# Optimization experiments

Hardware: AMD Instinct MI355X
Metric: run time of the kernel (lower is better)

## Reference

```python
import jax, jax.numpy as jnp
import numpy as np

B, L_SRC, H = 16, 2048, 1024


def setup_inputs() -> dict:
    key = jax.random.key(0)
    ks = jax.random.split(key, 12)
    s = 1.0 / np.sqrt(H)
    return {
        "query": jax.random.normal(ks[0], (B, 1, H), jnp.float32),
        "states": jax.random.normal(ks[1], (B, L_SRC, H), jnp.float32),
        "states_features": jax.random.normal(ks[2], (B, L_SRC, H), jnp.float32),
        "coverage": jax.random.uniform(ks[3], (B, L_SRC, 1), jnp.float32),
        "source_mask": jax.random.randint(ks[4], (B, L_SRC), 0, 2, jnp.int32),
        "is_coverage": 1,
        "Wq": jax.random.normal(ks[5], (H, H), jnp.float32) * s,
        "bq": jax.random.normal(ks[6], (H,), jnp.float32) * s,
        "Wc": jax.random.normal(ks[7], (1, H), jnp.float32) * s,
        "v": jax.random.normal(ks[8], (H, 1), jnp.float32) * s,
        "Wout": jax.random.normal(ks[9], (H, 2 * H), jnp.float32) * s,
        "bout": jax.random.normal(ks[10], (H,), jnp.float32) * s,
    }


def reference(query, states, states_features, coverage, source_mask, is_coverage,
              Wq, bq, Wc, v, Wout, bout):
    # query: (B,1,H); states/states_features: (B,L,H); coverage: (B,L,1)
    query_features = query @ Wq.T + bq                       # (B,1,H), broadcasts over L
    total = query_features + states_features                 # (B,L,H)
    if is_coverage:
        total = total + coverage @ Wc                        # Linear(1,H), no bias
    alignments = jnp.tanh(total) @ v                         # (B,L,1)
    mask = source_mask.astype(bool)[:, :, None]              # (B,L,1)
    alignments = jnp.where(mask, alignments, -jnp.inf)
    align_vectors = jax.nn.softmax(alignments, axis=1)       # softmax over L_src
    c = jnp.einsum('bls,blh->bsh', align_vectors, states)    # (B,1,H)
    concat_c = jnp.concatenate([c, query], axis=2)           # (B,1,2H)
    attn_h = concat_c @ Wout.T + bout                         # (B,1,H)
    new_coverage = coverage + align_vectors
    return attn_h, new_coverage, align_vectors
```

## Files before the change

kernel.cpp:

```cpp
#include <hip/hip_runtime.h>
#include <cfloat>

#define HD 1024
#define LS 2048
#define NB 16
#define LCHUNK 64
#define LPER   (LS / LCHUNK)

struct f4 { float x, y, z, w; };

__device__ inline f4 ld4(const float* p) { return *reinterpret_cast<const f4*>(p); }

__device__ inline float ftanh(float x) {
    x = fminf(10.f, fmaxf(-10.f, x));
    float t = __expf(2.f * x);
    return 1.f - 2.f * __builtin_amdgcn_rcpf(t + 1.f);
}

__device__ inline float dotTanh(const f4& s, const f4& q, const f4& wc, const f4& v, float covs) {
    return ftanh(s.x + q.x + covs * wc.x) * v.x
         + ftanh(s.y + q.y + covs * wc.y) * v.y
         + ftanh(s.z + q.z + covs * wc.z) * v.z
         + ftanh(s.w + q.w + covs * wc.w) * v.w;
}

__device__ inline float waveReduce(float v) {
    #pragma unroll
    for (int off = 32; off; off >>= 1) v += __shfl_xor(v, off, 64);
    return v;
}

__global__ void qf_kernel(const float* __restrict__ query, const float* __restrict__ Wq,
                          const float* __restrict__ bq, float* __restrict__ qf) {
    int h = blockIdx.x;
    int tid = threadIdx.x;
    int wv = tid >> 6, lane = tid & 63;
    int k0 = tid * 4;
    f4 w = ld4(Wq + (size_t)h * HD + k0);
    __shared__ float red[4][NB];
    float acc[NB];
    #pragma unroll
    for (int b = 0; b < NB; ++b) {
        f4 q = ld4(query + b * HD + k0);
        acc[b] = w.x * q.x + w.y * q.y + w.z * q.z + w.w * q.w;
    }
    #pragma unroll
    for (int b = 0; b < NB; ++b) {
        float r = waveReduce(acc[b]);
        if (lane == 0) red[wv][b] = r;
    }
    __syncthreads();
    if (tid < NB) {
        float s = red[0][tid] + red[1][tid] + red[2][tid] + red[3][tid];
        qf[tid * HD + h] = s + bq[h];
    }
}

__global__ __launch_bounds__(256) void fusedEC_kernel(
    const float* __restrict__ sf, const float* __restrict__ qf,
    const float* __restrict__ Wc, const float* __restrict__ vv,
    const float* __restrict__ coverage, const int* __restrict__ mask,
    const int* __restrict__ is_cov_p, const float* __restrict__ states,
    float* __restrict__ e_out, float* __restrict__ cpart)
{
    int chunk = blockIdx.x;
    int b = blockIdx.y;
    int tid = threadIdx.x;
    int wv = tid >> 6, lane = tid & 63;
    int l4 = lane * 4;
    int base_row = b * LS + chunk * LPER;
    int row0 = base_row + wv * 8;

    __shared__ float e_loc[LPER];

    int covflag = *is_cov_p;
    int4 mk0 = *reinterpret_cast<const int4*>(mask + row0);
    int4 mk1 = *reinterpret_cast<const int4*>(mask + row0 + 4);
    bool m[8] = { mk0.x != 0, mk0.y != 0, mk0.z != 0, mk0.w != 0,
                  mk1.x != 0, mk1.y != 0, mk1.z != 0, mk1.w != 0 };
    float cov[8];
    #pragma unroll
    for (int r = 0; r < 8; ++r) cov[r] = (covflag && m[r]) ? coverage[row0 + r] : 0.f;

    const float* qfr = qf + b * HD + l4;
    const float* ps = sf + (size_t)row0 * HD + l4;
    float acc[8] = {0.f, 0.f, 0.f, 0.f, 0.f, 0.f, 0.f, 0.f};

    #pragma unroll
    for (int it = 0; it < 4; ++it) {
        int o = it * 256;
        f4 q  = ld4(qfr + o);
        f4 wc = ld4(Wc + o + l4);
        f4 vf = ld4(vv + o + l4);
        f4 s[8];
        #pragma unroll
        for (int r = 0; r < 8; ++r) if (m[r]) s[r] = ld4(ps + (size_t)r * HD + o);
        #pragma unroll
        for (int r = 0; r < 8; ++r) if (m[r]) acc[r] += dotTanh(s[r], q, wc, vf, cov[r]);
    }

    #pragma unroll
    for (int off = 32; off; off >>= 1) {
        #pragma unroll
        for (int r = 0; r < 8; ++r) acc[r] += __shfl_xor(acc[r], off, 64);
    }
    if (lane == 0) {
        float ev[8];
        #pragma unroll
        for (int r = 0; r < 8; ++r) ev[r] = m[r] ? acc[r] : -1e30f;
        f4 o0, o1;
        o0.x = ev[0]; o0.y = ev[1]; o0.z = ev[2]; o0.w = ev[3];
        o1.x = ev[4]; o1.y = ev[5]; o1.z = ev[6]; o1.w = ev[7];
        *reinterpret_cast<f4*>(e_out + row0) = o0;
        *reinterpret_cast<f4*>(e_out + row0 + 4) = o1;
        #pragma unroll
        for (int r = 0; r < 8; ++r) e_loc[wv * 8 + r] = ev[r];
    }
    __syncthreads();

    __shared__ float wq[LPER];
    __shared__ int ridx[LPER];
    __shared__ int snnz;
    if (tid < 64) {
        float ev = (tid < LPER) ? e_loc[tid] : -1e30f;
        float w = __expf(ev);
        unsigned long long bm = __ballot(w != 0.f);
        if (w != 0.f) {
            int pos = __popcll(bm & ((1ull << tid) - 1));
            wq[pos] = w;
            ridx[pos] = tid;
        }
        if (tid == 0) snnz = __popcll(bm);
    }
    __syncthreads();
    int nnz = snnz;
    int h0 = tid * 4;
    const float* sbase = states + (size_t)base_row * HD + h0;
    float ax = 0.f, ay = 0.f, az = 0.f, aw = 0.f;
    for (int i = 0; i < nnz; i += 4) {
        int j1 = i + 1, j2 = i + 2, j3 = i + 3;
        float w0 = wq[i];
        int   r0 = ridx[i];
        float w1 = (j1 < nnz) ? wq[j1] : 0.f;
        int   r1 = (j1 < nnz) ? ridx[j1] : r0;
        float w2 = (j2 < nnz) ? wq[j2] : 0.f;
        int   r2 = (j2 < nnz) ? ridx[j2] : r0;
        float w3 = (j3 < nnz) ? wq[j3] : 0.f;
        int   r3 = (j3 < nnz) ? ridx[j3] : r0;
        f4 s0 = ld4(sbase + ((size_t)r0 << 10));
        f4 s1 = ld4(sbase + ((size_t)r1 << 10));
        f4 s2 = ld4(sbase + ((size_t)r2 << 10));
        f4 s3 = ld4(sbase + ((size_t)r3 << 10));
        ax = fmaf(w0, s0.x, ax); ay = fmaf(w0, s0.y, ay); az = fmaf(w0, s0.z, az); aw = fmaf(w0, s0.w, aw);
        ax = fmaf(w1, s1.x, ax); ay = fmaf(w1, s1.y, ay); az = fmaf(w1, s1.z, az); aw = fmaf(w1, s1.w, aw);
        ax = fmaf(w2, s2.x, ax); ay = fmaf(w2, s2.y, ay); az = fmaf(w2, s2.z, az); aw = fmaf(w2, s2.w, aw);
        ax = fmaf(w3, s3.x, ax); ay = fmaf(w3, s3.y, ay); az = fmaf(w3, s3.z, az); aw = fmaf(w3, s3.w, aw);
    }
    f4 o; o.x = ax; o.y = ay; o.z = az; o.w = aw;
    *reinterpret_cast<f4*>(cpart + ((size_t)(b * LCHUNK + chunk)) * HD + h0) = o;
}

__global__ __launch_bounds__(1024) void mid_kernel(
    const float* __restrict__ e, const float* __restrict__ coverage,
    const float* __restrict__ cpart, float* __restrict__ scale,
    float* __restrict__ csum, float* __restrict__ out_align, float* __restrict__ out_newcov)
{
    __shared__ float redm[16], reds[16];
    __shared__ float red4[4][256];
    if (blockIdx.x < 16) {
        int b = blockIdx.x;
        int t = threadIdx.x;
        int wv = t >> 6, lane = t & 63;
        float v0 = e[b * LS + t];
        float v1 = e[b * LS + t + 1024];
        float mx = fmaxf(v0, v1);
        #pragma unroll
        for (int off = 32; off; off >>= 1) mx = fmaxf(mx, __shfl_xor(mx, off, 64));
        if (lane == 0) redm[wv] = mx;
        __syncthreads();
        mx = redm[0];
        #pragma unroll
        for (int i = 1; i < 16; ++i) mx = fmaxf(mx, redm[i]);
        float e0 = __expf(v0 - mx), e1 = __expf(v1 - mx);
        float s = e0 + e1;
        #pragma unroll
        for (int off = 32; off; off >>= 1) s += __shfl_xor(s, off, 64);
        if (lane == 0) reds[wv] = s;
        __syncthreads();
        s = 0.f;
        #pragma unroll
        for (int i = 0; i < 16; ++i) s += reds[i];
        float invZ = 1.f / s;
        if (t == 0) scale[b] = __expf(-mx) * invZ;
        int i0 = b * LS + t, i1 = i0 + 1024;
        float p0 = e0 * invZ, p1 = e1 * invZ;
        out_align[i0] = p0;
        out_align[i1] = p1;
        out_newcov[i0] = coverage[i0] + p0;
        out_newcov[i1] = coverage[i1] + p1;
    } else {
        int blk = blockIdx.x - 16;
        int tt = threadIdx.x & 255;
        int g = threadIdx.x >> 8;
        int elem = blk * 256 + tt;
        int b = elem >> 10, h = elem & 1023;
        const float* p = cpart + (((size_t)(b * LCHUNK + g * 16)) << 10) + h;
        float s = 0.f;
        #pragma unroll
        for (int ch = 0; ch < 16; ++ch) s += p[(size_t)ch << 10];
        red4[g][tt] = s;
        __syncthreads();
        if (g == 0) csum[elem] = red4[0][tt] + red4[1][tt] + red4[2][tt] + red4[3][tt];
    }
}

__global__ void out_kernel(const float* __restrict__ csum, const float* __restrict__ query,
                           const float* __restrict__ Wout, const float* __restrict__ bout,
                           const float* __restrict__ scale, float* __restrict__ attn) {
    int h = blockIdx.x;
    int tid = threadIdx.x;
    int wv = tid >> 6, lane = tid & 63;
    int j0 = tid * 8;
    const float* wr = Wout + (size_t)h * (2 * HD);
    f4 w0 = ld4(wr + j0);
    f4 w1 = ld4(wr + j0 + 4);
    const float* src = (j0 < HD) ? (csum + j0) : (query + j0 - HD);
    __shared__ float red[4][NB];
    float acc[NB];
    #pragma unroll
    for (int b = 0; b < NB; ++b) {
        f4 x0 = ld4(src + b * HD);
        f4 x1 = ld4(src + b * HD + 4);
        acc[b] = w0.x * x0.x + w0.y * x0.y + w0.z * x0.z + w0.w * x0.w
               + w1.x * x1.x + w1.y * x1.y + w1.z * x1.z + w1.w * x1.w;
    }
    #pragma unroll
    for (int b = 0; b < NB; ++b) {
        float r = waveReduce(acc[b]);
        if (lane == 0) red[wv][b] = r;
    }
    __syncthreads();
    if (tid < NB) {
        float cpartial = red[0][tid] + red[1][tid];
        float qpartial = red[2][tid] + red[3][tid];
        attn[tid * HD + h] = cpartial * scale[tid] + qpartial + bout[h];
    }
}

extern "C" void kernel_launch(void* const* d_in, const int* in_sizes, int n_in,
                              void* d_out, int out_size, void* d_ws, size_t ws_size,
                              hipStream_t stream) {
    const float* query    = (const float*)d_in[0];
    const float* states   = (const float*)d_in[1];
    const float* sf       = (const float*)d_in[2];
    const float* coverage = (const float*)d_in[3];
    const int*   mask     = (const int*)d_in[4];
    const int*   is_cov   = (const int*)d_in[5];
    const float* Wq       = (const float*)d_in[6];
    const float* bq       = (const float*)d_in[7];
    const float* Wc       = (const float*)d_in[8];
    const float* v        = (const float*)d_in[9];
    const float* Wout     = (const float*)d_in[10];
    const float* bout     = (const float*)d_in[11];

    float* out      = (float*)d_out;
    float* attn     = out;
    float* newcov   = out + 16384;
    float* alignout = out + 49152;

    float* w  = (float*)d_ws;
    float* qf      = w;
    float* e       = w + 16384;
    float* cpart   = w + 49152;
    float* scale   = w + 49152 + 1048576;
    float* csum    = scale + 16;

    qf_kernel<<<dim3(HD), dim3(256), 0, stream>>>(query, Wq, bq, qf);
    fusedEC_kernel<<<dim3(LCHUNK, NB), dim3(256), 0, stream>>>(
        sf, qf, Wc, v, coverage, mask, is_cov, states, e, cpart);
    mid_kernel<<<dim3(80), dim3(1024), 0, stream>>>(e, coverage, cpart, scale, csum, alignout, newcov);
    out_kernel<<<dim3(HD), dim3(256), 0, stream>>>(csum, query, Wout, bout, scale, attn);
}
```

Baseline: 54.87 us.

## Double the L-chunk grid, software-prefetch streamed rows with nontemporal loads

The fused energy/context kernel now runs 128 chunks of 16 rows per batch instead of 64 chunks of 32, so each wave handles 4 rows rather than 8. The per-row feature loads are software-pipelined one step ahead, and both the features and states streams use nontemporal loads. The aim is more blocks in flight and better latency hiding on the bandwidth-bound streaming pass. In exchange, the partial-context buffer doubles and the mid kernel's reduction over chunks gets longer.

```diff
diff --git a/kernel.cpp b/kernel.cpp
--- a/kernel.cpp
+++ b/kernel.cpp
@@ -4,12 +4,18 @@
 #define HD 1024
 #define LS 2048
 #define NB 16
-#define LCHUNK 64
-#define LPER   (LS / LCHUNK)
+#define NCH 128
+#define LPER (LS / NCH)
 
 struct f4 { float x, y, z, w; };
+typedef float v4f __attribute__((ext_vector_type(4)));
 
 __device__ inline f4 ld4(const float* p) { return *reinterpret_cast<const f4*>(p); }
+
+__device__ inline f4 ldnt4(const float* p) {
+    v4f v = __builtin_nontemporal_load(reinterpret_cast<const v4f*>(p));
+    f4 r; r.x = v.x; r.y = v.y; r.z = v.z; r.w = v.w; return r;
+}
 
 __device__ inline float ftanh(float x) {
     x = fminf(10.f, fmaxf(-10.f, x));
@@ -69,52 +75,66 @@
     int wv = tid >> 6, lane = tid & 63;
     int l4 = lane * 4;
     int base_row = b * LS + chunk * LPER;
-    int row0 = base_row + wv * 8;
+    int row0 = base_row + wv * 4;
 
     __shared__ float e_loc[LPER];
 
     int covflag = *is_cov_p;
-    int4 mk0 = *reinterpret_cast<const int4*>(mask + row0);
-    int4 mk1 = *reinterpret_cast<const int4*>(mask + row0 + 4);
-    bool m[8] = { mk0.x != 0, mk0.y != 0, mk0.z != 0, mk0.w != 0,
-                  mk1.x != 0, mk1.y != 0, mk1.z != 0, mk1.w != 0 };
-    float cov[8];
-    #pragma unroll
-    for (int r = 0; r < 8; ++r) cov[r] = (covflag && m[r]) ? coverage[row0 + r] : 0.f;
+    int4 mk = *reinterpret_cast<const int4*>(mask + row0);
+    bool m0 = mk.x != 0, m1 = mk.y != 0, m2 = mk.z != 0, m3 = mk.w != 0;
+    float cov0 = (covflag && m0) ? coverage[row0 + 0] : 0.f;
+    float cov1 = (covflag && m1) ? coverage[row0 + 1] : 0.f;
+    float cov2 = (covflag && m2) ? coverage[row0 + 2] : 0.f;
+    float cov3 = (covflag && m3) ? coverage[row0 + 3] : 0.f;
 
     const float* qfr = qf + b * HD + l4;
     const float* ps = sf + (size_t)row0 * HD + l4;
-    float acc[8] = {0.f, 0.f, 0.f, 0.f, 0.f, 0.f, 0.f, 0.f};
-
+    float a0 = 0.f, a1 = 0.f, a2 = 0.f, a3 = 0.f;
+
+    f4 sA0, sA1, sA2, sA3;
+    if (m0) sA0 = ldnt4(ps);
+    if (m1) sA1 = ldnt4(ps + HD);
+    if (m2) sA2 = ldnt4(ps + 2 * HD);
+    if (m3) sA3 = ldnt4(ps + 3 * HD);
     #pragma unroll
     for (int it = 0; it < 4; ++it) {
         int o = it * 256;
         f4 q  = ld4(qfr + o);
         f4 wc = ld4(Wc + o + l4);
         f4 vf = ld4(vv + o + l4);
-        f4 s[8];
-        #pragma unroll
-        for (int r = 0; r < 8; ++r) if (m[r]) s[r] = ld4(ps + (size_t)r * HD + o);
-        #pragma unroll
-        for (int r = 0; r < 8; ++r) if (m[r]) acc[r] += dotTanh(s[r], q, wc, vf, cov[r]);
+        f4 sB0, sB1, sB2, sB3;
+        if (it < 3) {
+            int on = o + 256;
+            if (m0) sB0 = ldnt4(ps + on);
+            if (m1) sB1 = ldnt4(ps + HD + on);
+            if (m2) sB2 = ldnt4(ps + 2 * HD + on);
+            if (m3) sB3 = ldnt4(ps + 3 * HD + on);
+        }
+        if (m0) a0 += dotTanh(sA0, q, wc, vf, cov0);
+        if (m1) a1 += dotTanh(sA1, q, wc, vf, cov1);
+        if (m2) a2 += dotTanh(sA2, q, wc, vf, cov2);
+        if (m3) a3 += dotTanh(sA3, q, wc, vf, cov3);
+        if (it < 3) { sA0 = sB0; sA1 = sB1; sA2 = sB2; sA3 = sB3; }
     }
 
     #pragma unroll
     for (int off = 32; off; off >>= 1) {
-        #pragma unroll
-        for (int r = 0; r < 8; ++r) acc[r] += __shfl_xor(acc[r], off, 64);
+        a0 += __shfl_xor(a0, off, 64);
+        a1 += __shfl_xor(a1, off, 64);
+        a2 += __shfl_xor(a2, off, 64);
+        a3 += __shfl_xor(a3, off, 64);
     }
     if (lane == 0) {
-        float ev[8];
-        #pragma unroll
-        for (int r = 0; r < 8; ++r) ev[r] = m[r] ? acc[r] : -1e30f;
-        f4 o0, o1;
-        o0.x = ev[0]; o0.y = ev[1]; o0.z = ev[2]; o0.w = ev[3];
-        o1.x = ev[4]; o1.y = ev[5]; o1.z = ev[6]; o1.w = ev[7];
-        *reinterpret_cast<f4*>(e_out + row0) = o0;
-        *reinterpret_cast<f4*>(e_out + row0 + 4) = o1;
-        #pragma unroll
-        for (int r = 0; r < 8; ++r) e_loc[wv * 8 + r] = ev[r];
+        f4 o;
+        o.x = m0 ? a0 : -1e30f;
+        o.y = m1 ? a1 : -1e30f;
+        o.z = m2 ? a2 : -1e30f;
+        o.w = m3 ? a3 : -1e30f;
+        *reinterpret_cast<f4*>(e_out + row0) = o;
+        e_loc[wv * 4 + 0] = o.x;
+        e_loc[wv * 4 + 1] = o.y;
+        e_loc[wv * 4 + 2] = o.z;
+        e_loc[wv * 4 + 3] = o.w;
     }
     __syncthreads();
 
@@ -147,17 +167,17 @@
         int   r2 = (j2 < nnz) ? ridx[j2] : r0;
         float w3 = (j3 < nnz) ? wq[j3] : 0.f;
         int   r3 = (j3 < nnz) ? ridx[j3] : r0;
-        f4 s0 = ld4(sbase + ((size_t)r0 << 10));
-        f4 s1 = ld4(sbase + ((size_t)r1 << 10));
-        f4 s2 = ld4(sbase + ((size_t)r2 << 10));
-        f4 s3 = ld4(sbase + ((size_t)r3 << 10));
+        f4 s0 = ldnt4(sbase + ((size_t)r0 << 10));
+        f4 s1 = ldnt4(sbase + ((size_t)r1 << 10));
+        f4 s2 = ldnt4(sbase + ((size_t)r2 << 10));
+        f4 s3 = ldnt4(sbase + ((size_t)r3 << 10));
         ax = fmaf(w0, s0.x, ax); ay = fmaf(w0, s0.y, ay); az = fmaf(w0, s0.z, az); aw = fmaf(w0, s0.w, aw);
         ax = fmaf(w1, s1.x, ax); ay = fmaf(w1, s1.y, ay); az = fmaf(w1, s1.z, az); aw = fmaf(w1, s1.w, aw);
         ax = fmaf(w2, s2.x, ax); ay = fmaf(w2, s2.y, ay); az = fmaf(w2, s2.z, az); aw = fmaf(w2, s2.w, aw);
         ax = fmaf(w3, s3.x, ax); ay = fmaf(w3, s3.y, ay); az = fmaf(w3, s3.z, az); aw = fmaf(w3, s3.w, aw);
     }
     f4 o; o.x = ax; o.y = ay; o.z = az; o.w = aw;
-    *reinterpret_cast<f4*>(cpart + ((size_t)(b * LCHUNK + chunk)) * HD + h0) = o;
+    *reinterpret_cast<f4*>(cpart + ((size_t)(b * NCH + chunk)) * HD + h0) = o;
 }
 
 __global__ __launch_bounds__(1024) void mid_kernel(
@@ -204,10 +224,10 @@
         int g = threadIdx.x >> 8;
         int elem = blk * 256 + tt;
         int b = elem >> 10, h = elem & 1023;
-        const float* p = cpart + (((size_t)(b * LCHUNK + g * 16)) << 10) + h;
+        const float* p = cpart + (((size_t)(b * NCH + g * 32)) << 10) + h;
         float s = 0.f;
         #pragma unroll
-        for (int ch = 0; ch < 16; ++ch) s += p[(size_t)ch << 10];
+        for (int ch = 0; ch < 32; ++ch) s += p[(size_t)ch << 10];
         red4[g][tt] = s;
         __syncthreads();
         if (g == 0) csum[elem] = red4[0][tt] + red4[1][tt] + red4[2][tt] + red4[3][tt];
@@ -272,11 +292,11 @@
     float* qf      = w;
     float* e       = w + 16384;
     float* cpart   = w + 49152;
-    float* scale   = w + 49152 + 1048576;
+    float* scale   = w + 49152 + 2097152;
     float* csum    = scale + 16;
 
     qf_kernel<<<dim3(HD), dim3(256), 0, stream>>>(query, Wq, bq, qf);
-    fusedEC_kernel<<<dim3(LCHUNK, NB), dim3(256), 0, stream>>>(
+    fusedEC_kernel<<<dim3(NCH, NB), dim3(256), 0, stream>>>(
         sf, qf, Wc, v, coverage, mask, is_cov, states, e, cpart);
     mid_kernel<<<dim3(80), dim3(1024), 0, stream>>>(e, coverage, cpart, scale, csum, alignout, newcov);
     out_kernel<<<dim3(HD), dim3(256), 0, stream>>>(csum, query, Wout, bout, scale, attn);
```

Measured after the change: 64.82 us. +18.1%, slower.
